# Kernel tuning notes

Hardware: AMD Instinct MI355X
Metric: run time of the kernel (lower is better)

The kernel has to match this reference:

```python
import jax, jax.numpy as jnp
import numpy as np
from jax import lax

sg = lax.stop_gradient

# (kernel, stride, pad, pool_k, pool_s) for the 7 conv blocks
CFG = [(16, 2, 7, 8, 4), (12, 2, 5, 4, 2), (9, 1, 4, 5, 2), (7, 1, 3, 4, 2),
       (5, 1, 2, 2, 2), (3, 1, 1, 2, 2), (3, 1, 1, 2, 2)]
W_SHAPES = [(8, 1, 16), (12, 8, 12), (32, 12, 9), (64, 32, 7),
            (64, 64, 5), (64, 64, 3), (72, 64, 3)]
CH = [8, 12, 32, 64, 64, 64, 72]


def bin_act(x):
    # forward: sign(x); backward: clipped-quadratic surrogate (STE)
    s = jnp.sign(x)
    le = (x < -1.0).astype(x.dtype)
    ri = (x >= 1.0).astype(x.dtype)
    cl = ((x >= -1.0) & (x < 0.0)).astype(x.dtype)
    cr = ((x >= 0.0) & (x < 1.0)).astype(x.dtype)
    out = cl * (2.0 + x) * x + cr * (2.0 - x) * x + ri - le
    return sg(s) + out - sg(out)


def bin_wei(w, axes):
    # forward: scale * sign(w) with scale = mean|w| (detached); backward through tanh (STE)
    scale = sg(jnp.mean(jnp.abs(w), axis=axes, keepdims=True))
    t = jnp.tanh(w)
    return sg(scale * jnp.sign(w)) + t - sg(t)


def conv1d(x, w, stride, pad):
    return lax.conv_general_dilated(x, w, (stride,), [(pad, pad)],
                                    dimension_numbers=('NCH', 'OIH', 'NCH'))


def maxpool1d(x, k, s):
    return lax.reduce_window(x, -jnp.inf, lax.max, (1, 1, k), (1, 1, s), 'VALID')


def batchnorm1d(x, gamma, beta, eps=1e-5):
    # training-mode BN: batch statistics over (N, L), biased variance
    m = jnp.mean(x, axis=(0, 2), keepdims=True)
    v = jnp.mean((x - m) ** 2, axis=(0, 2), keepdims=True)
    return gamma[None, :, None] * (x - m) / jnp.sqrt(v + eps) + beta[None, :, None]


def _forward(x, ws, gs, bs, wfc):
    for w, g, b, (k, s, p, pk, ps) in zip(ws, gs, bs, CFG):
        x = conv1d(x, bin_wei(w, (1, 2)), s, p)
        x = maxpool1d(x, pk, ps)
        x = batchnorm1d(x, g, b)
        x = bin_act(x)
    x = x.reshape(x.shape[0], -1)                 # [B, 72*3]
    return x @ bin_wei(wfc, (1,)).T               # [B, classCount]


def setup_inputs() -> dict:
    key = jax.random.key(0)
    ks = jax.random.split(key, 9)
    inp = {'x': jax.random.normal(ks[0], (2048, 1, 3600), dtype=jnp.float32)}
    for i, shp in enumerate(W_SHAPES):
        inp[f'w{i+1}'] = jax.random.uniform(ks[i + 1], shp, dtype=jnp.float32) * 0.32
        inp[f'g{i+1}'] = jnp.ones((CH[i],), jnp.float32)
        inp[f'b{i+1}'] = jnp.zeros((CH[i],), jnp.float32)
    inp['wfc'] = jax.random.uniform(ks[8], (5, 216), dtype=jnp.float32) * 0.32
    return inp


def reference(x, w1, w2, w3, w4, w5, w6, w7,
              g1, g2, g3, g4, g5, g6, g7,
              b1, b2, b3, b4, b5, b6, b7, wfc):
    ws = [w1, w2, w3, w4, w5, w6, w7]
    gs = [g1, g2, g3, g4, g5, g6, g7]
    bs = [b1, b2, b3, b4, b5, b6, b7]
    return _forward(x, ws, gs, bs, wfc)
```

## Files before the change

kernel.cpp:

```cpp
#include <hip/hip_runtime.h>
#include <math.h>
#include <stdint.h>

#define NBATCH 2048
#define NSLOT 32

struct Args {
    const float* x;
    const float* W[7];
    const float* G[7];
    const float* Bt[7];
    const float* WFC;
    float* out;
    float* bufA;
    float* bufB;
    double* stats;
    float* wsc;
    uint32_t* wmb;
};

__device__ __forceinline__ float signf(float v) {
    return (v > 0.f) ? 1.f : ((v < 0.f) ? -1.f : 0.f);
}

__global__ __launch_bounds__(256) void k_setup(Args a) {
    const int blk = blockIdx.x, tid = threadIdx.x;
    for (int i = blk * 256 + tid; i < NSLOT * 632; i += 391 * 256) a.stats[i] = 0.0;

    if (blk < 321 && tid < 64) {
        const int cum[9] = {0,8,20,52,116,180,244,316,321};
        const int per[8] = {16,96,108,224,320,192,192,216};
        const float* wsrc[8] = {a.W[0],a.W[1],a.W[2],a.W[3],a.W[4],a.W[5],a.W[6],a.WFC};
        int o = blk, L = 0;
        while (L < 7 && o >= cum[L + 1]) ++L;
        const int oo = o - cum[L], p = per[L];
        const float* wo = wsrc[L] + (size_t)oo * p;
        float s = 0.f;
        for (int i = tid; i < p; i += 64) s += fabsf(wo[i]);
        #pragma unroll
        for (int off = 32; off; off >>= 1) s += __shfl_down(s, off);
        if (tid == 0) a.wsc[o] = s / (float)p;
    }

    const int gid = (blk - 384) * 256 + tid;
    if (blk >= 384 && blk <= 388 && gid >= 0 && gid < 1176) {
        const int cum[5]  = {0,448,768,960,1176};
        const int cin[4]  = {32,64,64,64};
        const int kk[4]   = {7,5,3,3};
        const int wpp[4]  = {1,2,2,2};
        const int woff[4] = {356,804,1444,1828};
        const float* wsrc[4] = {a.W[3],a.W[4],a.W[5],a.W[6]};
        int L = 0;
        while (L < 3 && gid >= cum[L + 1]) ++L;
        const int idx = gid - cum[L];
        const int K = kk[L], CIN = cin[L], WPP = wpp[L];
        const int o = idx / K, k = idx - o * K;
        const float* w = wsrc[L];
        uint32_t m0 = 0, m1 = 0;
        for (int c = 0; c < CIN; ++c) {
            const float v = w[((size_t)o * CIN + c) * K + k];
            const uint32_t bit = (v < 0.f) ? 1u : 0u;
            int bp = c;
            if (CIN == 64) bp = 16 * (c & 3) + (c >> 2);
            else if (CIN == 32) bp = 8 * (c & 3) + (c >> 2);
            if (bp < 32) m0 |= bit << bp; else m1 |= bit << (bp - 32);
        }
        uint32_t* dst = a.wmb + woff[L] + (size_t)idx * WPP;
        dst[0] = m0;
        if (WPP == 2) dst[1] = m1;
    }

    if (blk == 389 && tid < 12) {
        const float* w = a.W[1];
        const int o = tid;
        #pragma unroll
        for (int g = 0; g < 3; ++g) {
            uint32_t word = 0;
            #pragma unroll
            for (int j = 0; j < 4; ++j) {
                const int k = 4 * g + j;
                uint32_t by = 0;
                #pragma unroll
                for (int c = 0; c < 8; ++c)
                    by |= (w[((size_t)o * 8 + c) * 12 + k] < 0.f ? 1u : 0u) << c;
                word |= by << (8 * j);
            }
            a.wmb[o * 3 + g] = word;
        }
    }
    if (blk == 390 && tid < 64) {
        const float* w = a.W[2];
        const int o = tid >> 1, ph = tid & 1;
        uint32_t mk[9];
        #pragma unroll
        for (int k = 0; k < 9; ++k) {
            uint32_t m = 0;
            #pragma unroll
            for (int c = 0; c < 12; ++c)
                m |= (w[((size_t)o * 12 + c) * 9 + k] < 0.f ? 1u : 0u) << c;
            mk[k] = m;
        }
        uint32_t wd[5];
        if (ph == 0) { wd[0]=mk[0]|(mk[1]<<16); wd[1]=mk[2]|(mk[3]<<16);
                       wd[2]=mk[4]|(mk[5]<<16); wd[3]=mk[6]|(mk[7]<<16); wd[4]=mk[8]; }
        else         { wd[0]=mk[0]<<16; wd[1]=mk[1]|(mk[2]<<16);
                       wd[2]=mk[3]|(mk[4]<<16); wd[3]=mk[5]|(mk[6]<<16); wd[4]=mk[7]|(mk[8]<<16); }
        #pragma unroll
        for (int g = 0; g < 5; ++g) a.wmb[36 + o * 10 + ph * 5 + g] = wd[g];
    }
}

__global__ __launch_bounds__(256) void k_conv1(Args a) {
    __shared__ float wgs[128];
    __shared__ double sred[16];
    const int n = blockIdx.x, tid = threadIdx.x, l = tid & 63;
    if (tid < 128) wgs[tid] = signf(a.W[0][tid]);
    if (tid < 16)  sred[tid] = 0.0;
    __syncthreads();
    const int r = tid;
    const float* xn = a.x + (size_t)n * 3600;
    float m0[8], m1[8];
    #pragma unroll
    for (int ch = 0; ch < 8; ++ch) { m0[ch] = 0.f; m1[ch] = 0.f; }
    if (r < 225) {
        float f[40];
        const int g0 = 16 * r - 8;
        #pragma unroll
        for (int b = 0; b < 10; ++b) {
            const int gg = g0 + 4 * b;
            if (gg >= 0 && gg <= 3596) {
                const float4 v = *(const float4*)(xn + gg);
                f[4*b] = v.x; f[4*b+1] = v.y; f[4*b+2] = v.z; f[4*b+3] = v.w;
            } else {
                f[4*b] = 0.f; f[4*b+1] = 0.f; f[4*b+2] = 0.f; f[4*b+3] = 0.f;
            }
        }
        #pragma unroll
        for (int ch = 0; ch < 8; ++ch) {
            float acc[12];
            #pragma unroll
            for (int j = 0; j < 12; ++j) acc[j] = 0.f;
            #pragma unroll
            for (int k = 0; k < 16; ++k) {
                const float wk = wgs[ch * 16 + k];
                #pragma unroll
                for (int j = 0; j < 12; ++j)
                    acc[j] = fmaf(f[2*j + 1 + k], wk, acc[j]);
            }
            const float lo  = fmaxf(fmaxf(acc[0], acc[1]), fmaxf(acc[2], acc[3]));
            const float mid = fmaxf(fmaxf(acc[4], acc[5]), fmaxf(acc[6], acc[7]));
            const float hi  = fmaxf(fmaxf(acc[8], acc[9]), fmaxf(acc[10], acc[11]));
            const float sc = a.wsc[ch];
            m0[ch] = fmaxf(lo, mid) * sc;
            m1[ch] = (r < 224) ? fmaxf(mid, hi) * sc : 0.f;
        }
        float* on = a.bufA + ((size_t)n * 449 + 2 * r) * 8;
        *(float4*)(on + 0) = make_float4(m0[0], m0[1], m0[2], m0[3]);
        *(float4*)(on + 4) = make_float4(m0[4], m0[5], m0[6], m0[7]);
        if (r < 224) {
            *(float4*)(on + 8)  = make_float4(m1[0], m1[1], m1[2], m1[3]);
            *(float4*)(on + 12) = make_float4(m1[4], m1[5], m1[6], m1[7]);
        }
    }
    #pragma unroll
    for (int ch = 0; ch < 8; ++ch) {
        double sS = (double)m0[ch] + (double)m1[ch];
        double s2 = (double)m0[ch] * m0[ch] + (double)m1[ch] * m1[ch];
        #pragma unroll
        for (int off = 32; off; off >>= 1) {
            sS += __shfl_down(sS, off);
            s2 += __shfl_down(s2, off);
        }
        if (l == 0) {
            atomicAdd(&sred[ch], sS);
            atomicAdd(&sred[8 + ch], s2);
        }
    }
    __syncthreads();
    if (tid < 16) {
        double* so = a.stats + (size_t)(n & (NSLOT - 1)) * 16;
        atomicAdd(&so[tid], sred[tid]);
    }
}

template <int CIN, int LIN, int O, int K, int STRIDE, int PAD,
          int PK, int PS, int LP, int WPP, int LPB, int NS, bool SF64>
__device__ __forceinline__ void bin_body(
    const float* __restrict__ xprev, const uint32_t* __restrict__ wm,
    const float* __restrict__ wsc, const float* __restrict__ wsc_prev,
    const double* __restrict__ stats_in,
    const float* __restrict__ gamma, const float* __restrict__ beta,
    const double cntInv, float* __restrict__ out, double* __restrict__ stats_out)
{
    constexpr int OL    = (O < 64) ? O : 64;
    constexpr int PO    = 64 / OL;
    constexpr int WPW   = 4 / NS;
    constexpr int SPAN  = (PK - 1) * STRIDE + K;
    constexpr int QLEN  = WPW * LPB * PS * STRIDE + SPAN;
    constexpr int XM64A =
        (WPP == 2)   ? (QLEN + 3)
      : (CIN == 8)   ? ((QLEN + 48) + 7) / 8
      : (CIN == 12)  ? ((2 * (QLEN + 10)) + 7) / 8
      : ((QLEN + 5) / 2 + 2);
    constexpr int F     = 2 * CIN;
    constexpr int FW    = (F > 64) ? 128 : 64;

    __shared__ uint64_t xmbuf[NS][XM64A];
    __shared__ long long foldU[4][FW];
    __shared__ int sS[4][O], sS2[4][O];

    const int tid  = threadIdx.x;
    const int wv   = tid >> 6;
    const int l    = tid & 63;
    const int sloc = wv / WPW;
    const int wvs  = wv % WPW;
    uint64_t* xm64 = xmbuf[sloc];
    uint32_t* xm32 = (uint32_t*)xm64;
    uint16_t* xm16 = (uint16_t*)xm64;
    uint8_t*  xm8  = (uint8_t*)xm64;

    const int n    = blockIdx.x * NS + sloc;
    const int lp0b = blockIdx.y * (WPW * LPB);
    const int lp1b = (lp0b + WPW * LPB < LP) ? lp0b + WPW * LPB : LP;
    const int q0raw = lp0b * PS * STRIDE - PAD;
    const int q0 = (q0raw > 0) ? q0raw : 0;
    const int q1raw = (lp1b - 1) * PS * STRIDE - PAD + SPAN;
    const int q1 = (q1raw < LIN) ? q1raw : LIN;
    int xbase;
    if constexpr (CIN == 8)       xbase = q0 & ~3;
    else if constexpr (CIN == 12) xbase = q0 - (q0 & 1);
    else if constexpr (WPP == 1)  xbase = q0 - ((q0 + (PAD & 1)) & 1);
    else                          xbase = q0;

    const int lp0 = lp0b + wvs * LPB;
    const int lp1 = (lp0 + LPB < lp1b) ? lp0 + LPB : lp1b;

    const float* xn = xprev + (size_t)n * LIN * CIN;

    {
        const long long* stI = (const long long*)stats_in;
        long long pa = 0, pb_ = 0;
        double da = 0.0;
        #pragma unroll
        for (int s8 = 0; s8 < 8; ++s8) {
            const int s = (wv << 3) + s8;
            if constexpr (SF64) {
                if (l < F) da += stats_in[s * F + l];
            } else {
                if (l < ((F < 64) ? F : 64)) pa += stI[s * F + l];
                if constexpr (F > 64) { if (l < F - 64) pb_ += stI[s * F + 64 + l]; }
            }
        }
        if constexpr (SF64) foldU[wv][l] = __double_as_longlong(da);
        else {
            foldU[wv][l] = pa;
            if constexpr (F > 64) foldU[wv][64 + l] = pb_;
        }
    }
    __syncthreads();
    float aA = 0.f, aB = 0.f;
    {
        double t0 = 0.0, t1 = 0.0;
        if constexpr (SF64) {
            double tot = 0.0;
            #pragma unroll
            for (int w = 0; w < 4; ++w) tot += __longlong_as_double(foldU[w][l]);
            t0 = tot;
            t1 = __shfl(tot, CIN + l);
        } else if constexpr (F > 64) {
            long long a0 = 0, a1 = 0;
            #pragma unroll
            for (int w = 0; w < 4; ++w) { a0 += foldU[w][l]; a1 += foldU[w][64 + l]; }
            t0 = (double)a0; t1 = (double)a1;
        } else {
            long long a0 = 0;
            #pragma unroll
            for (int w = 0; w < 4; ++w) a0 += foldU[w][l];
            const double tot = (double)a0;
            t0 = tot;
            t1 = __shfl(tot, CIN + l);
        }
        if (l < CIN) {
            double mean, E2;
            if constexpr (SF64) { mean = t0 * cntInv; E2 = t1 * cntInv; }
            else {
                const double w = (double)wsc_prev[l];
                mean = w * t0 * cntInv; E2 = w * w * t1 * cntInv;
            }
            const double var = E2 - mean * mean;
            const double inv = 1.0 / sqrt(var + 1e-5);
            const double av  = (double)gamma[l] * inv;
            aA = (float)av;
            aB = (float)((double)beta[l] - mean * av);
        }
    }

    if constexpr (CIN == 64) {
        const int sub = l & 15, grp = l >> 4;
        const float a0 = __shfl(aA, 4*sub),     b0 = __shfl(aB, 4*sub);
        const float a1 = __shfl(aA, 4*sub + 1), b1 = __shfl(aB, 4*sub + 1);
        const float a2 = __shfl(aA, 4*sub + 2), b2 = __shfl(aB, 4*sub + 2);
        const float a3 = __shfl(aA, 4*sub + 3), b3 = __shfl(aB, 4*sub + 3);
        for (int pb = q0 + wvs * 4; pb < q1; pb += WPW * 4) {
            const int pos = pb + grp;
            const bool valid = pos < q1;
            const float4 v = *(const float4*)(xn + (size_t)(valid ? pos : q0) * 64 + 4*sub);
            const unsigned long long bal0 = __ballot(valid && (fmaf(a0, v.x, b0) < 0.f));
            const unsigned long long bal1 = __ballot(valid && (fmaf(a1, v.y, b1) < 0.f));
            const unsigned long long bal2 = __ballot(valid && (fmaf(a2, v.z, b2) < 0.f));
            const unsigned long long bal3 = __ballot(valid && (fmaf(a3, v.w, b3) < 0.f));
            if (l < 4 && pb + l < q1) {
                const uint64_t m = ((bal0 >> (16*l)) & 0xFFFFull)
                                 | (((bal1 >> (16*l)) & 0xFFFFull) << 16)
                                 | (((bal2 >> (16*l)) & 0xFFFFull) << 32)
                                 | (((bal3 >> (16*l)) & 0xFFFFull) << 48);
                xm64[pb + l - xbase] = m;
            }
        }
    } else if constexpr (CIN == 32) {
        const int sub = l & 7, grp = l >> 3;
        const float a0 = __shfl(aA, 4*sub),     b0 = __shfl(aB, 4*sub);
        const float a1 = __shfl(aA, 4*sub + 1), b1 = __shfl(aB, 4*sub + 1);
        const float a2 = __shfl(aA, 4*sub + 2), b2 = __shfl(aB, 4*sub + 2);
        const float a3 = __shfl(aA, 4*sub + 3), b3 = __shfl(aB, 4*sub + 3);
        for (int pb = q0 + wvs * 8; pb < q1; pb += WPW * 8) {
            const int pos = pb + grp;
            const bool valid = pos < q1;
            const float4 v = *(const float4*)(xn + (size_t)(valid ? pos : q0) * 32 + 4*sub);
            const unsigned long long bal0 = __ballot(valid && (fmaf(a0, v.x, b0) < 0.f));
            const unsigned long long bal1 = __ballot(valid && (fmaf(a1, v.y, b1) < 0.f));
            const unsigned long long bal2 = __ballot(valid && (fmaf(a2, v.z, b2) < 0.f));
            const unsigned long long bal3 = __ballot(valid && (fmaf(a3, v.w, b3) < 0.f));
            if (l < 8 && pb + l < q1) {
                const uint32_t m = (uint32_t)((bal0 >> (8*l)) & 0xFFull)
                                 | ((uint32_t)((bal1 >> (8*l)) & 0xFFull) << 8)
                                 | ((uint32_t)((bal2 >> (8*l)) & 0xFFull) << 16)
                                 | ((uint32_t)((bal3 >> (8*l)) & 0xFFull) << 24);
                xm32[pb + l - xbase] = m;
            }
        }
    } else if constexpr (CIN == 8) {
        const int sub = l & 1, grp = l >> 1;
        const float a0 = __shfl(aA, 4*sub),     b0 = __shfl(aB, 4*sub);
        const float a1 = __shfl(aA, 4*sub + 1), b1 = __shfl(aB, 4*sub + 1);
        const float a2 = __shfl(aA, 4*sub + 2), b2 = __shfl(aB, 4*sub + 2);
        const float a3 = __shfl(aA, 4*sub + 3), b3 = __shfl(aB, 4*sub + 3);
        for (int pb = q0 + wvs * 32; pb < q1; pb += WPW * 32) {
            const int pos = pb + grp;
            const bool valid = pos < q1;
            const float4 v = *(const float4*)(xn + (size_t)(valid ? pos : q0) * 8 + 4*sub);
            const unsigned long long bal0 = __ballot(valid && (fmaf(a0, v.x, b0) < 0.f));
            const unsigned long long bal1 = __ballot(valid && (fmaf(a1, v.y, b1) < 0.f));
            const unsigned long long bal2 = __ballot(valid && (fmaf(a2, v.z, b2) < 0.f));
            const unsigned long long bal3 = __ballot(valid && (fmaf(a3, v.w, b3) < 0.f));
            if (l < 32 && pb + l < q1) {
                const uint32_t t0 = (uint32_t)((bal0 >> (2*l)) & 3ull);
                const uint32_t t1 = (uint32_t)((bal1 >> (2*l)) & 3ull);
                const uint32_t t2 = (uint32_t)((bal2 >> (2*l)) & 3ull);
                const uint32_t t3 = (uint32_t)((bal3 >> (2*l)) & 3ull);
                const uint32_t m = (t0 & 1) | ((t1 & 1) << 1) | ((t2 & 1) << 2) | ((t3 & 1) << 3)
                                 | ((t0 >> 1) << 4) | ((t1 >> 1) << 5) | ((t2 >> 1) << 6) | ((t3 >> 1) << 7);
                xm8[pb + l - xbase] = (uint8_t)m;
            }
        }
    } else {
        constexpr int PPW = 64 / CIN;
        const int pw = l / CIN, c = l - pw * CIN;
        const float myA = __shfl(aA, c), myB = __shfl(aB, c);
        const bool lact = (pw < PPW);
        for (int pb = q0 + wvs * PPW; pb < q1; pb += WPW * PPW) {
            const int pos = pb + pw;
            const bool act = lact && (pos < q1);
            float v = 0.f;
            if (act) v = fmaf(myA, xn[(size_t)pb * CIN + l], myB);
            const unsigned long long bal = __ballot(act && (v < 0.f));
            if (act && c == 0) {
                const uint32_t mk = (uint32_t)((bal >> (pw * CIN)) & ((1u << CIN) - 1));
                xm16[pos - xbase] = (uint16_t)mk;
            }
        }
    }
    __syncthreads();

    float* on = out + (size_t)n * LP * O;

    if constexpr (WPP == 2) {
        const uint64_t* wmp = (const uint64_t*)wm;
        uint64_t wr[K];
        #pragma unroll
        for (int k = 0; k < K; ++k) wr[k] = wmp[l * K + k];
        uint64_t wr2[K];
        const int oo2 = 64 + ((O > 64 && l < O - 64) ? l : 0);
        if constexpr (O > 64) {
            #pragma unroll
            for (int k = 0; k < K; ++k) wr2[k] = wmp[oo2 * K + k];
        }
        const float myws  = wsc[l];
        const float myws2 = (O > 64 && l < O - 64) ? wsc[64 + l] : 0.f;
        int accS = 0, accS2 = 0, accSb = 0, accS2b = 0;

        for (int lp = lp0; lp < lp1; ++lp) {
            const int lo = lp * PS * STRIDE - PAD;
            int m = -1000000, m2 = -1000000;
            if (lo >= 0 && lo + SPAN <= LIN) {
                uint64_t tw[SPAN];
                #pragma unroll
                for (int t = 0; t < SPAN; ++t) tw[t] = xm64[lo - xbase + t];
                #pragma unroll
                for (int j = 0; j < PK; ++j) {
                    int p = 0;
                    #pragma unroll
                    for (int k = 0; k < K; ++k)
                        p += __popcll(tw[j * STRIDE + k] ^ wr[k]);
                    m = max(m, CIN * K - 2 * p);
                    if constexpr (O > 64) {
                        int p2 = 0;
                        #pragma unroll
                        for (int k = 0; k < K; ++k)
                            p2 += __popcll(tw[j * STRIDE + k] ^ wr2[k]);
                        m2 = max(m2, CIN * K - 2 * p2);
                    }
                }
            } else {
                #pragma unroll
                for (int j = 0; j < PK; ++j) {
                    const int base = lo + j * STRIDE;
                    int p = 0, nv = 0, p2 = 0;
                    #pragma unroll
                    for (int k = 0; k < K; ++k) {
                        const int q = base + k;
                        if (q >= 0 && q < LIN) {
                            ++nv;
                            const uint64_t xv = xm64[q - xbase];
                            p += __popcll(xv ^ wr[k]);
                            if constexpr (O > 64) p2 += __popcll(xv ^ wr2[k]);
                        }
                    }
                    m = max(m, CIN * nv - 2 * p);
                    if constexpr (O > 64) m2 = max(m2, CIN * nv - 2 * p2);
                }
            }
            on[lp * O + l] = (float)m * myws;
            accS += m; accS2 += m * m;
            if constexpr (O > 64) {
                if (l < O - 64) {
                    on[lp * O + 64 + l] = (float)m2 * myws2;
                    accSb += m2; accS2b += m2 * m2;
                }
            }
        }
        sS[wv][l] = accS; sS2[wv][l] = accS2;
        if constexpr (O > 64) {
            if (l < O - 64) { sS[wv][64 + l] = accSb; sS2[wv][64 + l] = accS2b; }
            else if (l >= O - 64) {  }
        }
    } else if constexpr (CIN == 8) {
        const int po = l / OL, oo = l - po * OL;
        const bool cact = (po < PO);
        const float myws = cact ? wsc[oo] : 0.f;
        const int osel = cact ? oo : 0;
        const uint32_t wr0 = wm[osel*3], wr1 = wm[osel*3+1], wr2 = wm[osel*3+2];
        uint32_t wb[12];
        #pragma unroll
        for (int k = 0; k < 12; ++k)
            wb[k] = ((k < 4 ? wr0 : (k < 8 ? wr1 : wr2)) >> (8 * (k & 3))) & 255u;
        const uint32_t* xw = (const uint32_t*)xm64;
        int accS = 0, accS2 = 0;

        for (int lp = lp0 + po; lp < lp1; lp += PO) {
            const int lo = lp * PS * STRIDE - PAD;
            int m = -1000000;
            if (lo >= 0 && lo + SPAN <= LIN) {
                const int bb = lo - xbase;
                const int w0 = bb >> 2;
                uint32_t tw[6];
                #pragma unroll
                for (int i = 0; i < 6; ++i) tw[i] = xw[w0 + i];
                #pragma unroll
                for (int j = 0; j < PK; ++j) {
                    const int wo = (j + 1) >> 1;
                    uint32_t e0, e1, e2;
                    if (j & 1) {
                        e0 = (tw[wo]   >> 8) | (tw[wo+1] << 24);
                        e1 = (tw[wo+1] >> 8) | (tw[wo+2] << 24);
                        e2 = (tw[wo+2] >> 8) | (tw[wo+3] << 24);
                    } else {
                        e0 = (tw[wo]   >> 24) | (tw[wo+1] << 8);
                        e1 = (tw[wo+1] >> 24) | (tw[wo+2] << 8);
                        e2 = (tw[wo+2] >> 24) | (tw[wo+3] << 8);
                    }
                    const int p = __popc(e0 ^ wr0) + __popc(e1 ^ wr1) + __popc(e2 ^ wr2);
                    m = max(m, 96 - 2 * p);
                }
            } else {
                #pragma unroll
                for (int j = 0; j < PK; ++j) {
                    const int base = lo + j * STRIDE;
                    int p = 0, nv = 0;
                    #pragma unroll
                    for (int k = 0; k < 12; ++k) {
                        const int q = base + k;
                        if (q >= 0 && q < LIN) { ++nv; p += __popc((uint32_t)xm8[q - xbase] ^ wb[k]); }
                    }
                    m = max(m, 8 * nv - 2 * p);
                }
            }
            if (cact) {
                on[lp * O + oo] = (float)m * myws;
                accS += m; accS2 += m * m;
            }
        }
        int t = accS, t2 = accS2;
        #pragma unroll
        for (int g = 1; g < PO; ++g) {
            t  += __shfl(accS,  l + g * OL);
            t2 += __shfl(accS2, l + g * OL);
        }
        if (l < OL) { sS[wv][l] = t; sS2[wv][l] = t2; }
        else if (l < O) { sS[wv][l] = 0; sS2[wv][l] = 0; }
    } else if constexpr (CIN == 12) {
        const int po = l / OL, oo = l - po * OL;
        const bool cact = (po < PO);
        const float myws = cact ? wsc[oo] : 0.f;
        const int osel = cact ? oo : 0;
        uint32_t wE[5], wO[5];
        #pragma unroll
        for (int g = 0; g < 5; ++g) { wE[g] = wm[osel*10 + g]; wO[g] = wm[osel*10 + 5 + g]; }
        uint32_t we16[9];
        we16[0]=wE[0]&0xFFFFu; we16[1]=wE[0]>>16; we16[2]=wE[1]&0xFFFFu; we16[3]=wE[1]>>16;
        we16[4]=wE[2]&0xFFFFu; we16[5]=wE[2]>>16; we16[6]=wE[3]&0xFFFFu; we16[7]=wE[3]>>16;
        we16[8]=wE[4]&0xFFFFu;
        const uint32_t* xw = (const uint32_t*)xm64;
        int accS = 0, accS2 = 0;

        for (int lp = lp0 + po; lp < lp1; lp += PO) {
            const int lo = lp * PS * STRIDE - PAD;
            int m = -1000000;
            if (lo >= 0 && lo + SPAN <= LIN) {
                const int s0 = (lo - xbase) >> 1;
                uint32_t tw[7];
                #pragma unroll
                for (int i = 0; i < 7; ++i) tw[i] = xw[s0 + i];
                #pragma unroll
                for (int j = 0; j < PK; ++j) {
                    const int o_ = j >> 1;
                    int p;
                    if (j & 1)
                        p = __popc((tw[o_] & 0xFFFF0000u) ^ wO[0]) + __popc(tw[o_+1] ^ wO[1])
                          + __popc(tw[o_+2] ^ wO[2]) + __popc(tw[o_+3] ^ wO[3])
                          + __popc(tw[o_+4] ^ wO[4]);
                    else
                        p = __popc(tw[o_] ^ wE[0]) + __popc(tw[o_+1] ^ wE[1])
                          + __popc(tw[o_+2] ^ wE[2]) + __popc(tw[o_+3] ^ wE[3])
                          + __popc((tw[o_+4] & 0xFFFFu) ^ wE[4]);
                    m = max(m, 108 - 2 * p);
                }
            } else {
                #pragma unroll
                for (int j = 0; j < PK; ++j) {
                    const int base = lo + j * STRIDE;
                    int p = 0, nv = 0;
                    #pragma unroll
                    for (int k = 0; k < 9; ++k) {
                        const int q = base + k;
                        if (q >= 0 && q < LIN) { ++nv; p += __popc((uint32_t)xm16[q - xbase] ^ we16[k]); }
                    }
                    m = max(m, 12 * nv - 2 * p);
                }
            }
            if (cact) {
                on[lp * O + oo] = (float)m * myws;
                accS += m; accS2 += m * m;
            }
        }
        int t = accS, t2 = accS2;
        #pragma unroll
        for (int g = 1; g < PO; ++g) {
            t  += __shfl(accS,  l + g * OL);
            t2 += __shfl(accS2, l + g * OL);
        }
        if (l < OL) { sS[wv][l] = t; sS2[wv][l] = t2; }
    } else {
        const int po = l / OL, oo = l - po * OL;
        const bool cact = (po < PO);
        const float myws = cact ? wsc[oo] : 0.f;
        uint32_t wr[K];
        #pragma unroll
        for (int k = 0; k < K; ++k) wr[k] = wm[(cact ? oo : 0) * K + k];
        int accS = 0, accS2 = 0;

        constexpr int PAIRS = (SPAN + 1) / 2;
        for (int lp = lp0 + po; lp < lp1; lp += PO) {
            const int lo = lp * PS * STRIDE - PAD;
            int m = -1000000;
            if (lo >= 0 && lo + SPAN <= LIN) {
                uint32_t tw[PAIRS * 2];
                const int e0 = (lo - xbase) >> 1;
                #pragma unroll
                for (int i = 0; i < PAIRS; ++i) {
                    const uint64_t u64v = xm64[e0 + i];
                    tw[2 * i]     = (uint32_t)u64v;
                    tw[2 * i + 1] = (uint32_t)(u64v >> 32);
                }
                #pragma unroll
                for (int j = 0; j < PK; ++j) {
                    int p = 0;
                    #pragma unroll
                    for (int k = 0; k < K; ++k)
                        p += __popc(tw[j * STRIDE + k] ^ wr[k]);
                    m = max(m, CIN * K - 2 * p);
                }
            } else {
                #pragma unroll
                for (int j = 0; j < PK; ++j) {
                    const int base = lo + j * STRIDE;
                    int p = 0, nv = 0;
                    #pragma unroll
                    for (int k = 0; k < K; ++k) {
                        const int q = base + k;
                        if (q >= 0 && q < LIN) { ++nv; p += __popc(xm32[q - xbase] ^ wr[k]); }
                    }
                    m = max(m, CIN * nv - 2 * p);
                }
            }
            if (cact) {
                on[lp * O + oo] = (float)m * myws;
                accS += m; accS2 += m * m;
            }
        }
        int t = accS, t2 = accS2;
        #pragma unroll
        for (int g = 1; g < PO; ++g) {
            t  += __shfl(accS,  l + g * OL);
            t2 += __shfl(accS2, l + g * OL);
        }
        if (l < OL) { sS[wv][l] = t; sS2[wv][l] = t2; }
    }
    __syncthreads();

    const int slot = ((NS == 1) ? n : (int)blockIdx.x) & (NSLOT - 1);
    unsigned long long* soU =
        (unsigned long long*)stats_out + (size_t)slot * 2 * O;
    for (int t = tid; t < 2 * O; t += 256) {
        int tot;
        if (t < O) tot = sS[0][t] + sS[1][t] + sS[2][t] + sS[3][t];
        else { const int f = t - O; tot = sS2[0][f] + sS2[1][f] + sS2[2][f] + sS2[3][f]; }
        atomicAdd(&soU[t], (unsigned long long)(long long)tot);
    }
}

#define BIN_PARAMS \
    const float* __restrict__ xprev, const uint32_t* __restrict__ wm, \
    const float* __restrict__ wsc, const float* __restrict__ wsc_prev, \
    const double* __restrict__ stats_in, \
    const float* __restrict__ gamma, const float* __restrict__ beta, \
    const double cntInv, float* __restrict__ out, double* __restrict__ stats_out
#define BIN_ARGS xprev, wm, wsc, wsc_prev, stats_in, gamma, beta, cntInv, out, stats_out

__global__ __launch_bounds__(256) void k_bin2(BIN_PARAMS) { bin_body< 8,449,12,12,2,5,4,2,111,1,28,1,true >(BIN_ARGS); }
__global__ __launch_bounds__(256) void k_bin3(BIN_PARAMS) { bin_body<12,111,32, 9,1,4,5,2, 54,1,14,1,false>(BIN_ARGS); }
__global__ __launch_bounds__(256) void k_bin4(BIN_PARAMS) { bin_body<32, 54,64, 7,1,3,4,2, 26,1, 7,1,false>(BIN_ARGS); }
__global__ __launch_bounds__(256) void k_bin5(BIN_PARAMS) { bin_body<64, 26,64, 5,1,2,2,2, 13,2, 7,2,false>(BIN_ARGS); }
__global__ __launch_bounds__(256) void k_bin6(BIN_PARAMS) { bin_body<64, 13,64, 3,1,1,2,2,  6,2, 3,2,false>(BIN_ARGS); }
__global__ __launch_bounds__(256) void k_bin7(BIN_PARAMS) { bin_body<64,  6,72, 3,1,1,2,2,  3,2, 2,2,false>(BIN_ARGS); }

__global__ __launch_bounds__(256) void k_fc(Args a) {
    const int n = blockIdx.x * 4 + (int)(threadIdx.x >> 6);
    const int l = (int)(threadIdx.x & 63);
    const long long* st = (const long long*)(a.stats + 15616);
    long long s = 0, s2 = 0, sb = 0, s2b = 0;
    #pragma unroll 4
    for (int sl = 0; sl < NSLOT; ++sl) {
        s  += st[sl * 144 + l];
        s2 += st[sl * 144 + 72 + l];
        if (l < 8) {
            sb  += st[sl * 144 + 64 + l];
            s2b += st[sl * 144 + 72 + 64 + l];
        }
    }
    float aA0, aB0, aA1 = 0.f, aB1 = 0.f;
    {
        const double w = (double)a.wsc[244 + l];
        const double mean = w * (double)s / 6144.0;
        const double E2   = w * w * (double)s2 / 6144.0;
        const double var  = E2 - mean * mean;
        const double inv  = 1.0 / sqrt(var + 1e-5);
        const double aa   = (double)a.G[6][l] * inv;
        aA0 = (float)aa; aB0 = (float)((double)a.Bt[6][l] - mean * aa);
    }
    if (l < 8) {
        const double w = (double)a.wsc[244 + 64 + l];
        const double mean = w * (double)sb / 6144.0;
        const double E2   = w * w * (double)s2b / 6144.0;
        const double var  = E2 - mean * mean;
        const double inv  = 1.0 / sqrt(var + 1e-5);
        const double aa   = (double)a.G[6][64 + l] * inv;
        aA1 = (float)aa; aB1 = (float)((double)a.Bt[6][64 + l] - mean * aa);
    }
    const float* p7 = a.bufA + (size_t)n * 216;
    float acc[5] = {0.f, 0.f, 0.f, 0.f, 0.f};
    #pragma unroll
    for (int j = 0; j < 4; ++j) {
        const int i = l + 64 * j;
        const int ic = (i < 216) ? i : 215;
        const int c = ic / 3, lp = ic - 3 * c;
        float aa = __shfl(aA0, c);
        float bb = __shfl(aB0, c);
        const float aaH = __shfl(aA1, c - 64);
        const float bbH = __shfl(aB1, c - 64);
        if (c >= 64) { aa = aaH; bb = bbH; }
        if (i < 216) {
            const float av = signf(fmaf(aa, p7[lp * 72 + c], bb));
            #pragma unroll
            for (int o = 0; o < 5; ++o)
                acc[o] += av * signf(a.WFC[o * 216 + i]);
        }
    }
    #pragma unroll
    for (int o = 0; o < 5; ++o) {
        float v = acc[o];
        #pragma unroll
        for (int off = 32; off; off >>= 1) v += __shfl_down(v, off);
        if (l == 0) a.out[(size_t)n * 5 + o] = v * a.wsc[316 + o];
    }
}

extern "C" void kernel_launch(void* const* d_in, const int* in_sizes, int n_in,
                              void* d_out, int out_size, void* d_ws, size_t ws_size,
                              hipStream_t stream) {
    Args a;
    a.x = (const float*)d_in[0];
    for (int i = 0; i < 7; ++i) {
        a.W[i]  = (const float*)d_in[1 + 3 * i];
        a.G[i]  = (const float*)d_in[2 + 3 * i];
        a.Bt[i] = (const float*)d_in[3 + 3 * i];
    }
    a.WFC = (const float*)d_in[22];
    a.out = (float*)d_out;

    char* ws = (char*)d_ws;
    a.bufA  = (float*)ws;
    a.bufB  = (float*)(ws + 29425664);
    a.stats = (double*)(ws + 43057152);
    a.wsc   = (float*)(ws + 43218944);
    a.wmb   = (uint32_t*)d_out;

    k_setup<<<391, 256, 0, stream>>>(a);
    k_conv1<<<NBATCH, 256, 0, stream>>>(a);
    k_bin2<<<dim3(NBATCH, 1), 256, 0, stream>>>(
        a.bufA, a.wmb + 0, a.wsc + 8, a.wsc, a.stats + 0, a.G[0], a.Bt[0],
        1.0/919552.0, a.bufB, a.stats + 512);
    k_bin3<<<dim3(NBATCH, 1), 256, 0, stream>>>(
        a.bufB, a.wmb + 36, a.wsc + 20, a.wsc + 8, a.stats + 512, a.G[1], a.Bt[1],
        1.0/227328.0, a.bufA, a.stats + 1280);
    k_bin4<<<dim3(NBATCH, 1), 256, 0, stream>>>(
        a.bufA, a.wmb + 356, a.wsc + 52, a.wsc + 20, a.stats + 1280, a.G[2], a.Bt[2],
        1.0/110592.0, a.bufB, a.stats + 3328);
    k_bin5<<<dim3(NBATCH / 2, 1), 256, 0, stream>>>(
        a.bufB, a.wmb + 804, a.wsc + 116, a.wsc + 52, a.stats + 3328, a.G[3], a.Bt[3],
        1.0/53248.0, a.bufA, a.stats + 7424);
    k_bin6<<<dim3(NBATCH / 2, 1), 256, 0, stream>>>(
        a.bufA, a.wmb + 1444, a.wsc + 180, a.wsc + 116, a.stats + 7424, a.G[4], a.Bt[4],
        1.0/26624.0, a.bufB, a.stats + 11520);
    k_bin7<<<dim3(NBATCH / 2, 1), 256, 0, stream>>>(
        a.bufB, a.wmb + 1828, a.wsc + 244, a.wsc + 180, a.stats + 11520, a.G[5], a.Bt[5],
        1.0/12288.0, a.bufA, a.stats + 15616);
    k_fc<<<NBATCH / 4, 256, 0, stream>>>(a);
}
```

Measured before the change: 254.9 us.

## Stage conv1 input in LDS and drop spatial block split in binary conv

Conv1 now loads each sample's 3600-float input into shared memory with coalesced float4 loads and zero-pads the halo, so threads read overlapping windows from LDS instead of issuing redundant global loads. The binary conv kernel drops the blockIdx.y spatial split: each block covers the whole length, the base offset becomes a compile-time constant, and the binarize and popcount loops use fixed trip counts with unroll pragmas. This cuts index arithmetic and halo recomputation but removes length-wise parallelism, and it is only correct if the launch grid was already one block along y.

```diff
diff --git a/kernel.cpp b/kernel.cpp
--- a/kernel.cpp
+++ b/kernel.cpp
@@ -111,29 +111,32 @@
 }
 
 __global__ __launch_bounds__(256) void k_conv1(Args a) {
+    __shared__ float xs[3624];
     __shared__ float wgs[128];
     __shared__ double sred[16];
     const int n = blockIdx.x, tid = threadIdx.x, l = tid & 63;
     if (tid < 128) wgs[tid] = signf(a.W[0][tid]);
     if (tid < 16)  sred[tid] = 0.0;
+    if (tid < 8)   xs[tid] = 0.f;
+    else if (tid < 24) xs[3600 + tid] = 0.f;
+    const float* xn = a.x + (size_t)n * 3600;
+    #pragma unroll
+    for (int i = 0; i < 4; ++i) {
+        const int idx = tid + 256 * i;
+        if (idx < 900) *(float4*)&xs[8 + 4 * idx] = *(const float4*)(xn + 4 * idx);
+    }
     __syncthreads();
     const int r = tid;
-    const float* xn = a.x + (size_t)n * 3600;
     float m0[8], m1[8];
     #pragma unroll
     for (int ch = 0; ch < 8; ++ch) { m0[ch] = 0.f; m1[ch] = 0.f; }
     if (r < 225) {
         float f[40];
-        const int g0 = 16 * r - 8;
-        #pragma unroll
-        for (int b = 0; b < 10; ++b) {
-            const int gg = g0 + 4 * b;
-            if (gg >= 0 && gg <= 3596) {
-                const float4 v = *(const float4*)(xn + gg);
-                f[4*b] = v.x; f[4*b+1] = v.y; f[4*b+2] = v.z; f[4*b+3] = v.w;
-            } else {
-                f[4*b] = 0.f; f[4*b+1] = 0.f; f[4*b+2] = 0.f; f[4*b+3] = 0.f;
-            }
+        const int g0 = 16 * r;
+        #pragma unroll
+        for (int b = 0; b < 20; ++b) {
+            const float2 v = *(const float2*)&xs[g0 + 2 * b];
+            f[2*b] = v.x; f[2*b+1] = v.y;
         }
         #pragma unroll
         for (int ch = 0; ch < 8; ++ch) {
@@ -204,6 +207,8 @@
       : ((QLEN + 5) / 2 + 2);
     constexpr int F     = 2 * CIN;
     constexpr int FW    = (F > 64) ? 128 : 64;
+    constexpr int XBASE = (CIN == 8 || CIN == 12) ? 0
+                        : (WPP == 1) ? -(PAD & 1) : 0;
 
     __shared__ uint64_t xmbuf[NS][XM64A];
     __shared__ long long foldU[4][FW];
@@ -219,21 +224,9 @@
     uint16_t* xm16 = (uint16_t*)xm64;
     uint8_t*  xm8  = (uint8_t*)xm64;
 
-    const int n    = blockIdx.x * NS + sloc;
-    const int lp0b = blockIdx.y * (WPW * LPB);
-    const int lp1b = (lp0b + WPW * LPB < LP) ? lp0b + WPW * LPB : LP;
-    const int q0raw = lp0b * PS * STRIDE - PAD;
-    const int q0 = (q0raw > 0) ? q0raw : 0;
-    const int q1raw = (lp1b - 1) * PS * STRIDE - PAD + SPAN;
-    const int q1 = (q1raw < LIN) ? q1raw : LIN;
-    int xbase;
-    if constexpr (CIN == 8)       xbase = q0 & ~3;
-    else if constexpr (CIN == 12) xbase = q0 - (q0 & 1);
-    else if constexpr (WPP == 1)  xbase = q0 - ((q0 + (PAD & 1)) & 1);
-    else                          xbase = q0;
-
-    const int lp0 = lp0b + wvs * LPB;
-    const int lp1 = (lp0 + LPB < lp1b) ? lp0 + LPB : lp1b;
+    const int n   = blockIdx.x * NS + sloc;
+    const int lp0 = wvs * LPB;
+    const int lp1 = (lp0 + LPB < LP) ? lp0 + LPB : LP;
 
     const float* xn = xprev + (size_t)n * LIN * CIN;
 
@@ -296,87 +289,103 @@
     }
 
     if constexpr (CIN == 64) {
+        constexpr int STP = WPW * 4;
+        constexpr int MAXIT = (LIN + STP - 1) / STP;
         const int sub = l & 15, grp = l >> 4;
         const float a0 = __shfl(aA, 4*sub),     b0 = __shfl(aB, 4*sub);
         const float a1 = __shfl(aA, 4*sub + 1), b1 = __shfl(aB, 4*sub + 1);
         const float a2 = __shfl(aA, 4*sub + 2), b2 = __shfl(aB, 4*sub + 2);
         const float a3 = __shfl(aA, 4*sub + 3), b3 = __shfl(aB, 4*sub + 3);
-        for (int pb = q0 + wvs * 4; pb < q1; pb += WPW * 4) {
+        #pragma unroll
+        for (int it = 0; it < MAXIT; ++it) {
+            const int pb = wvs * 4 + it * STP;
             const int pos = pb + grp;
-            const bool valid = pos < q1;
-            const float4 v = *(const float4*)(xn + (size_t)(valid ? pos : q0) * 64 + 4*sub);
+            const bool valid = pos < LIN;
+            const float4 v = *(const float4*)(xn + (size_t)(valid ? pos : 0) * 64 + 4*sub);
             const unsigned long long bal0 = __ballot(valid && (fmaf(a0, v.x, b0) < 0.f));
             const unsigned long long bal1 = __ballot(valid && (fmaf(a1, v.y, b1) < 0.f));
             const unsigned long long bal2 = __ballot(valid && (fmaf(a2, v.z, b2) < 0.f));
             const unsigned long long bal3 = __ballot(valid && (fmaf(a3, v.w, b3) < 0.f));
-            if (l < 4 && pb + l < q1) {
+            if (l < 4 && pb + l < LIN) {
                 const uint64_t m = ((bal0 >> (16*l)) & 0xFFFFull)
                                  | (((bal1 >> (16*l)) & 0xFFFFull) << 16)
                                  | (((bal2 >> (16*l)) & 0xFFFFull) << 32)
                                  | (((bal3 >> (16*l)) & 0xFFFFull) << 48);
-                xm64[pb + l - xbase] = m;
+                xm64[pb + l - XBASE] = m;
             }
         }
     } else if constexpr (CIN == 32) {
+        constexpr int STP = WPW * 8;
+        constexpr int MAXIT = (LIN + STP - 1) / STP;
         const int sub = l & 7, grp = l >> 3;
         const float a0 = __shfl(aA, 4*sub),     b0 = __shfl(aB, 4*sub);
         const float a1 = __shfl(aA, 4*sub + 1), b1 = __shfl(aB, 4*sub + 1);
         const float a2 = __shfl(aA, 4*sub + 2), b2 = __shfl(aB, 4*sub + 2);
         const float a3 = __shfl(aA, 4*sub + 3), b3 = __shfl(aB, 4*sub + 3);
-        for (int pb = q0 + wvs * 8; pb < q1; pb += WPW * 8) {
+        #pragma unroll
+        for (int it = 0; it < MAXIT; ++it) {
+            const int pb = wvs * 8 + it * STP;
             const int pos = pb + grp;
-            const bool valid = pos < q1;
-            const float4 v = *(const float4*)(xn + (size_t)(valid ? pos : q0) * 32 + 4*sub);
+            const bool valid = pos < LIN;
+            const float4 v = *(const float4*)(xn + (size_t)(valid ? pos : 0) * 32 + 4*sub);
             const unsigned long long bal0 = __ballot(valid && (fmaf(a0, v.x, b0) < 0.f));
             const unsigned long long bal1 = __ballot(valid && (fmaf(a1, v.y, b1) < 0.f));
             const unsigned long long bal2 = __ballot(valid && (fmaf(a2, v.z, b2) < 0.f));
             const unsigned long long bal3 = __ballot(valid && (fmaf(a3, v.w, b3) < 0.f));
-            if (l < 8 && pb + l < q1) {
+            if (l < 8 && pb + l < LIN) {
                 const uint32_t m = (uint32_t)((bal0 >> (8*l)) & 0xFFull)
                                  | ((uint32_t)((bal1 >> (8*l)) & 0xFFull) << 8)
                                  | ((uint32_t)((bal2 >> (8*l)) & 0xFFull) << 16)
                                  | ((uint32_t)((bal3 >> (8*l)) & 0xFFull) << 24);
-                xm32[pb + l - xbase] = m;
+                xm32[pb + l - XBASE] = m;
             }
         }
     } else if constexpr (CIN == 8) {
+        constexpr int STP = WPW * 32;
+        constexpr int MAXIT = (LIN + STP - 1) / STP;
         const int sub = l & 1, grp = l >> 1;
         const float a0 = __shfl(aA, 4*sub),     b0 = __shfl(aB, 4*sub);
         const float a1 = __shfl(aA, 4*sub + 1), b1 = __shfl(aB, 4*sub + 1);
         const float a2 = __shfl(aA, 4*sub + 2), b2 = __shfl(aB, 4*sub + 2);
         const float a3 = __shfl(aA, 4*sub + 3), b3 = __shfl(aB, 4*sub + 3);
-        for (int pb = q0 + wvs * 32; pb < q1; pb += WPW * 32) {
+        #pragma unroll
+        for (int it = 0; it < MAXIT; ++it) {
+            const int pb = wvs * 32 + it * STP;
             const int pos = pb + grp;
-            const bool valid = pos < q1;
-            const float4 v = *(const float4*)(xn + (size_t)(valid ? pos : q0) * 8 + 4*sub);
+            const bool valid = pos < LIN;
+            const float4 v = *(const float4*)(xn + (size_t)(valid ? pos : 0) * 8 + 4*sub);
             const unsigned long long bal0 = __ballot(valid && (fmaf(a0, v.x, b0) < 0.f));
             const unsigned long long bal1 = __ballot(valid && (fmaf(a1, v.y, b1) < 0.f));
             const unsigned long long bal2 = __ballot(valid && (fmaf(a2, v.z, b2) < 0.f));
             const unsigned long long bal3 = __ballot(valid && (fmaf(a3, v.w, b3) < 0.f));
-            if (l < 32 && pb + l < q1) {
+            if (l < 32 && pb + l < LIN) {
                 const uint32_t t0 = (uint32_t)((bal0 >> (2*l)) & 3ull);
                 const uint32_t t1 = (uint32_t)((bal1 >> (2*l)) & 3ull);
                 const uint32_t t2 = (uint32_t)((bal2 >> (2*l)) & 3ull);
                 const uint32_t t3 = (uint32_t)((bal3 >> (2*l)) & 3ull);
                 const uint32_t m = (t0 & 1) | ((t1 & 1) << 1) | ((t2 & 1) << 2) | ((t3 & 1) << 3)
                                  | ((t0 >> 1) << 4) | ((t1 >> 1) << 5) | ((t2 >> 1) << 6) | ((t3 >> 1) << 7);
-                xm8[pb + l - xbase] = (uint8_t)m;
+                xm8[pb + l - XBASE] = (uint8_t)m;
             }
         }
     } else {
         constexpr int PPW = 64 / CIN;
+        constexpr int STP = WPW * PPW;
+        constexpr int MAXIT = (LIN + STP - 1) / STP;
         const int pw = l / CIN, c = l - pw * CIN;
         const float myA = __shfl(aA, c), myB = __shfl(aB, c);
         const bool lact = (pw < PPW);
-        for (int pb = q0 + wvs * PPW; pb < q1; pb += WPW * PPW) {
+        #pragma unroll
+        for (int it = 0; it < MAXIT; ++it) {
+            const int pb = wvs * PPW + it * STP;
             const int pos = pb + pw;
-            const bool act = lact && (pos < q1);
+            const bool act = lact && (pos < LIN) && (pb < LIN);
             float v = 0.f;
             if (act) v = fmaf(myA, xn[(size_t)pb * CIN + l], myB);
             const unsigned long long bal = __ballot(act && (v < 0.f));
             if (act && c == 0) {
                 const uint32_t mk = (uint32_t)((bal >> (pw * CIN)) & ((1u << CIN) - 1));
-                xm16[pos - xbase] = (uint16_t)mk;
+                xm16[pos - XBASE] = (uint16_t)mk;
             }
         }
     }
@@ -399,60 +408,63 @@
         const float myws2 = (O > 64 && l < O - 64) ? wsc[64 + l] : 0.f;
         int accS = 0, accS2 = 0, accSb = 0, accS2b = 0;
 
-        for (int lp = lp0; lp < lp1; ++lp) {
-            const int lo = lp * PS * STRIDE - PAD;
-            int m = -1000000, m2 = -1000000;
-            if (lo >= 0 && lo + SPAN <= LIN) {
-                uint64_t tw[SPAN];
-                #pragma unroll
-                for (int t = 0; t < SPAN; ++t) tw[t] = xm64[lo - xbase + t];
-                #pragma unroll
-                for (int j = 0; j < PK; ++j) {
-                    int p = 0;
+        #pragma unroll
+        for (int li = 0; li < LPB; ++li) {
+            const int lp = lp0 + li;
+            if (lp < lp1) {
+                const int lo = lp * PS * STRIDE - PAD;
+                int m = -1000000, m2 = -1000000;
+                if (lo >= 0 && lo + SPAN <= LIN) {
+                    uint64_t tw[SPAN];
                     #pragma unroll
-                    for (int k = 0; k < K; ++k)
-                        p += __popcll(tw[j * STRIDE + k] ^ wr[k]);
-                    m = max(m, CIN * K - 2 * p);
-                    if constexpr (O > 64) {
-                        int p2 = 0;
+                    for (int t = 0; t < SPAN; ++t) tw[t] = xm64[lo - XBASE + t];
+                    #pragma unroll
+                    for (int j = 0; j < PK; ++j) {
+                        int p = 0;
                         #pragma unroll
                         for (int k = 0; k < K; ++k)
-                            p2 += __popcll(tw[j * STRIDE + k] ^ wr2[k]);
-                        m2 = max(m2, CIN * K - 2 * p2);
-                    }
-                }
-            } else {
-                #pragma unroll
-                for (int j = 0; j < PK; ++j) {
-                    const int base = lo + j * STRIDE;
-                    int p = 0, nv = 0, p2 = 0;
-                    #pragma unroll
-                    for (int k = 0; k < K; ++k) {
-                        const int q = base + k;
-                        if (q >= 0 && q < LIN) {
-                            ++nv;
-                            const uint64_t xv = xm64[q - xbase];
-                            p += __popcll(xv ^ wr[k]);
-                            if constexpr (O > 64) p2 += __popcll(xv ^ wr2[k]);
+                            p += __popcll(tw[j * STRIDE + k] ^ wr[k]);
+                        m = max(m, CIN * K - 2 * p);
+                        if constexpr (O > 64) {
+                            int p2 = 0;
+                            #pragma unroll
+                            for (int k = 0; k < K; ++k)
+                                p2 += __popcll(tw[j * STRIDE + k] ^ wr2[k]);
+                            m2 = max(m2, CIN * K - 2 * p2);
                         }
                     }
-                    m = max(m, CIN * nv - 2 * p);
-                    if constexpr (O > 64) m2 = max(m2, CIN * nv - 2 * p2);
-                }
-            }
-            on[lp * O + l] = (float)m * myws;
-            accS += m; accS2 += m * m;
-            if constexpr (O > 64) {
-                if (l < O - 64) {
-                    on[lp * O + 64 + l] = (float)m2 * myws2;
-                    accSb += m2; accS2b += m2 * m2;
+                } else {
+                    #pragma unroll
+                    for (int j = 0; j < PK; ++j) {
+                        const int base = lo + j * STRIDE;
+                        int p = 0, nv = 0, p2 = 0;
+                        #pragma unroll
+                        for (int k = 0; k < K; ++k) {
+                            const int q = base + k;
+                            if (q >= 0 && q < LIN) {
+                                ++nv;
+                                const uint64_t xv = xm64[q - XBASE];
+                                p += __popcll(xv ^ wr[k]);
+                                if constexpr (O > 64) p2 += __popcll(xv ^ wr2[k]);
+                            }
+                        }
+                        m = max(m, CIN * nv - 2 * p);
+                        if constexpr (O > 64) m2 = max(m2, CIN * nv - 2 * p2);
+                    }
+                }
+                on[lp * O + l] = (float)m * myws;
+                accS += m; accS2 += m * m;
+                if constexpr (O > 64) {
+                    if (l < O - 64) {
+                        on[lp * O + 64 + l] = (float)m2 * myws2;
+                        accSb += m2; accS2b += m2 * m2;
+                    }
                 }
             }
         }
         sS[wv][l] = accS; sS2[wv][l] = accS2;
         if constexpr (O > 64) {
             if (l < O - 64) { sS[wv][64 + l] = accSb; sS2[wv][64 + l] = accS2b; }
-            else if (l >= O - 64) {  }
         }
     } else if constexpr (CIN == 8) {
         const int po = l / OL, oo = l - po * OL;
@@ -467,11 +479,12 @@
         const uint32_t* xw = (const uint32_t*)xm64;
         int accS = 0, accS2 = 0;
 
+        #pragma unroll 2
         for (int lp = lp0 + po; lp < lp1; lp += PO) {
             const int lo = lp * PS * STRIDE - PAD;
             int m = -1000000;
             if (lo >= 0 && lo + SPAN <= LIN) {
-                const int bb = lo - xbase;
+                const int bb = lo - XBASE;
                 const int w0 = bb >> 2;
                 uint32_t tw[6];
                 #pragma unroll
@@ -500,7 +513,7 @@
                     #pragma unroll
                     for (int k = 0; k < 12; ++k) {
                         const int q = base + k;
-                        if (q >= 0 && q < LIN) { ++nv; p += __popc((uint32_t)xm8[q - xbase] ^ wb[k]); }
+                        if (q >= 0 && q < LIN) { ++nv; p += __popc((uint32_t)xm8[q - XBASE] ^ wb[k]); }
                     }
                     m = max(m, 8 * nv - 2 * p);
                 }
@@ -533,11 +546,12 @@
         const uint32_t* xw = (const uint32_t*)xm64;
         int accS = 0, accS2 = 0;
 
+        #pragma unroll 2
         for (int lp = lp0 + po; lp < lp1; lp += PO) {
             const int lo = lp * PS * STRIDE - PAD;
             int m = -1000000;
             if (lo >= 0 && lo + SPAN <= LIN) {
-                const int s0 = (lo - xbase) >> 1;
+                const int s0 = (lo - XBASE) >> 1;
                 uint32_t tw[7];
                 #pragma unroll
                 for (int i = 0; i < 7; ++i) tw[i] = xw[s0 + i];
@@ -563,7 +577,7 @@
                     #pragma unroll
                     for (int k = 0; k < 9; ++k) {
                         const int q = base + k;
-                        if (q >= 0 && q < LIN) { ++nv; p += __popc((uint32_t)xm16[q - xbase] ^ we16[k]); }
+                        if (q >= 0 && q < LIN) { ++nv; p += __popc((uint32_t)xm16[q - XBASE] ^ we16[k]); }
                     }
                     m = max(m, 12 * nv - 2 * p);
                 }
@@ -590,12 +604,13 @@
         int accS = 0, accS2 = 0;
 
         constexpr int PAIRS = (SPAN + 1) / 2;
+        #pragma unroll 2
         for (int lp = lp0 + po; lp < lp1; lp += PO) {
             const int lo = lp * PS * STRIDE - PAD;
             int m = -1000000;
             if (lo >= 0 && lo + SPAN <= LIN) {
                 uint32_t tw[PAIRS * 2];
-                const int e0 = (lo - xbase) >> 1;
+                const int e0 = (lo - XBASE) >> 1;
                 #pragma unroll
                 for (int i = 0; i < PAIRS; ++i) {
                     const uint64_t u64v = xm64[e0 + i];
@@ -618,7 +633,7 @@
                     #pragma unroll
                     for (int k = 0; k < K; ++k) {
                         const int q = base + k;
-                        if (q >= 0 && q < LIN) { ++nv; p += __popc(xm32[q - xbase] ^ wr[k]); }
+                        if (q >= 0 && q < LIN) { ++nv; p += __popc(xm32[q - XBASE] ^ wr[k]); }
                     }
                     m = max(m, CIN * nv - 2 * p);
                 }
```

Result: no change. 259.7 us (+1.9%).
